# Kernel tuning notes

Measured on AMD Instinct MI355X. Metric: run time of the kernel, lower is better.

The kernel has to match this reference:

```python
import jax, jax.numpy as jnp
import numpy as np
from jax import lax


def ternarize(w):
    # TWN-style ternarization: threshold delta = 0.7*mean|w|, scale alpha =
    # mean |w| over surviving entries; straight-through in backward.
    aw = jnp.abs(w)
    delta = 0.7 * jnp.mean(aw)
    mask = (aw > delta).astype(w.dtype)
    alpha = jnp.sum(aw * mask) / jnp.maximum(jnp.sum(mask), 1.0)
    q = alpha * jnp.sign(w) * mask
    return w + lax.stop_gradient(q - w)


def conv2d(x, w, b):
    # x: [N,C,H,W], w: [O,I,kh,kw]
    y = lax.conv_general_dilated(x, w, window_strides=(1, 1), padding='VALID',
                                 dimension_numbers=('NCHW', 'OIHW', 'NCHW'))
    return y + b[None, :, None, None]


def maxpool2(x):
    return lax.reduce_window(x, -jnp.inf, lax.max,
                             window_dimensions=(1, 1, 2, 2),
                             window_strides=(1, 1, 2, 2), padding='VALID')


def setup_inputs() -> dict:
    key = jax.random.key(0)
    ks = jax.random.split(key, 11)
    n_classes = 10
    x = jax.random.normal(ks[0], (1024, 1, 32, 32), dtype=jnp.float32)
    # Kaiming-ish scaled params
    w1 = jax.random.normal(ks[1], (32, 1, 5, 5), jnp.float32) * (1.0 / np.sqrt(1 * 25))
    b1 = jnp.zeros((32,), jnp.float32)
    w2 = jax.random.normal(ks[2], (64, 32, 5, 5), jnp.float32) * (1.0 / np.sqrt(32 * 25))
    b2 = jnp.zeros((64,), jnp.float32)
    w3 = jax.random.normal(ks[3], (120, 64, 5, 5), jnp.float32) * (1.0 / np.sqrt(64 * 25))
    b3 = jnp.zeros((120,), jnp.float32)
    fw1 = jax.random.normal(ks[4], (84, 120), jnp.float32) * (1.0 / np.sqrt(120))
    fb1 = jnp.zeros((84,), jnp.float32)
    fw2 = jax.random.normal(ks[5], (n_classes, 84), jnp.float32) * (1.0 / np.sqrt(84))
    fb2 = jnp.zeros((n_classes,), jnp.float32)
    return {"x": x, "w1": w1, "b1": b1, "w2": w2, "b2": b2,
            "w3": w3, "b3": b3, "fw1": fw1, "fb1": fb1, "fw2": fw2, "fb2": fb2}


def reference(x, w1, b1, w2, b2, w3, b3, fw1, fb1, fw2, fb2):
    h = jnp.tanh(conv2d(x, ternarize(w1), b1))   # [N,32,28,28]
    h = maxpool2(h)                              # [N,32,14,14]
    h = jnp.tanh(conv2d(h, ternarize(w2), b2))   # [N,64,10,10]
    h = maxpool2(h)                              # [N,64,5,5]
    h = jnp.tanh(conv2d(h, ternarize(w3), b3))   # [N,120,1,1]
    h = h.reshape(h.shape[0], -1)                # [N,120]
    h = jnp.tanh(h @ ternarize(fw1).T + fb1)     # [N,84]
    logits = h @ ternarize(fw2).T + fb2          # [N,n_classes]
    probs = jax.nn.softmax(logits, axis=1)
    return (logits, probs)
```

## Files before the change

kernel.cpp:

```cpp
#include <hip/hip_runtime.h>
#include <hip/hip_bf16.h>
#include <math.h>


typedef __attribute__((ext_vector_type(8))) short bf16x8;
typedef __attribute__((ext_vector_type(4))) float f32x4;

static const size_t OFF_PB    = 0;
static const size_t OFF_Q1T   = 256;
static const size_t OFF_W2B   = 1056;
static const size_t OFF_W3B   = 26656;
static const size_t OFF_FW1T  = 129056;
static const size_t OFF_FW2T  = 139136;
static const size_t OFF_P2B   = 139976;
static const size_t OFF_H3    = 959176;

#define BPT 16

__device__ __forceinline__ ushort f2bf(float v) {
    unsigned u = __float_as_uint(v);
    unsigned r = (u + 0x7FFFu + ((u >> 16) & 1u)) >> 16;
    return (ushort)r;
}

__device__ __forceinline__ float tanh_fast(float x) {
    float e = __expf(-2.0f * fabsf(x));
    float r = 1.0f - 2.0f * e / (1.0f + e);
    return copysignf(r, x);
}

__device__ __forceinline__ void tensor_select(int tensor,
        const float* w1, const float* w2, const float* w3,
        const float* fw1, const float* fw2,
        const float*& src, int& O, int& K) {
    switch (tensor) {
        case 0: src = w1;  O = 32;  K = 25;   break;
        case 1: src = w2;  O = 64;  K = 800;  break;
        case 2: src = w3;  O = 120; K = 1600; break;
        case 3: src = fw1; O = 84;  K = 120;  break;
        default: src = fw2; O = 10; K = 84;   break;
    }
}

__device__ __forceinline__ float block_sum_256(float v, float* sbuf) {
    #pragma unroll
    for (int off = 32; off > 0; off >>= 1) v += __shfl_down(v, off);
    const int wid = threadIdx.x >> 6;
    if ((threadIdx.x & 63) == 0) sbuf[wid] = v;
    __syncthreads();
    return sbuf[0] + sbuf[1] + sbuf[2] + sbuf[3];
}

__device__ __forceinline__ float alpha_of(const float* pb, int tensor) {
    float s1 = 0.f, c = 0.f;
    #pragma unroll
    for (int i = 0; i < BPT; ++i) {
        s1 += pb[80 + tensor * BPT + i];
        c  += pb[160 + tensor * BPT + i];
    }
    return s1 / fmaxf(c, 1.0f);
}

__global__ __launch_bounds__(256)
void tern_pass1(const float* w1, const float* w2, const float* w3,
                const float* fw1, const float* fw2, float* pb) {
    __shared__ float sbuf[4];
    const int tensor = blockIdx.x / BPT;
    const int blk    = blockIdx.x % BPT;
    const float* src; int O, K;
    tensor_select(tensor, w1, w2, w3, fw1, fw2, src, O, K);
    const int n = O * K;
    float s = 0.f;
    for (int i = blk * 256 + threadIdx.x; i < n; i += BPT * 256)
        s += fabsf(src[i]);
    s = block_sum_256(s, sbuf);
    if (threadIdx.x == 0) pb[tensor * BPT + blk] = s;
}

__global__ __launch_bounds__(256)
void tern_pass2(const float* w1, const float* w2, const float* w3,
                const float* fw1, const float* fw2,
                float* q1t, ushort* w2b, ushort* w3b,
                float* fw1t, float* fw2t, float* pb) {
    __shared__ float sbuf[4];
    const int tensor = blockIdx.x / BPT;
    const int blk    = blockIdx.x % BPT;
    const float* src; int O, K;
    tensor_select(tensor, w1, w2, w3, fw1, fw2, src, O, K);
    const int n = O * K;
    float tot = 0.f;
    #pragma unroll
    for (int i = 0; i < BPT; ++i) tot += pb[tensor * BPT + i];
    const float delta = 0.7f * tot / (float)n;

    const ushort BP = 0x3F80u, BN = 0xBF80u;
    float s1 = 0.f, cnt = 0.f;

    if (tensor == 2) {
        for (int i = blk * 256 + threadIdx.x; i < 128 * 1600; i += BPT * 256) {
            ushort qb = 0;
            if (i < n) {
                float w = src[i];
                float aw = fabsf(w);
                if (aw > delta) { s1 += aw; cnt += 1.f; qb = (w > 0.f) ? BP : BN; }
            }
            w3b[i] = qb;
        }
    } else if (tensor == 1) {
        for (int i = blk * 256 + threadIdx.x; i < n; i += BPT * 256) {
            float w = src[i];
            float aw = fabsf(w);
            ushort qb = 0;
            if (aw > delta) { s1 += aw; cnt += 1.f; qb = (w > 0.f) ? BP : BN; }
            int oc = i / 800;
            int r  = i - oc * 800;
            int ic = r / 25;
            int tap = r - ic * 25;
            w2b[oc * 800 + tap * 32 + ic] = qb;
        }
    } else {
        float* dst = (tensor == 0) ? q1t : (tensor == 3) ? fw1t : fw2t;
        for (int i = blk * 256 + threadIdx.x; i < n; i += BPT * 256) {
            float w = src[i];
            float aw = fabsf(w);
            float q = 0.f;
            if (aw > delta) { s1 += aw; cnt += 1.f; q = (w > 0.f) ? 1.f : -1.f; }
            int o = i / K;
            int k = i - o * K;
            dst[k * O + o] = q;
        }
    }
    s1 = block_sum_256(s1, sbuf);
    __syncthreads();
    cnt = block_sum_256(cnt, sbuf);
    if (threadIdx.x == 0) {
        pb[80 + tensor * BPT + blk]  = s1;
        pb[160 + tensor * BPT + blk] = cnt;
    }
}

template<int TBASE, int TCNT>
__device__ __forceinline__ void conv2_phase(
        const ushort* __restrict__ w2b, const ushort* sxt,
        int n0, int mt0, int lane, f32x4 acc[4][2]) {
    const int col = lane & 15, quad = lane >> 4;
    bf16x8 bfr[TCNT][2];
    #pragma unroll
    for (int i = 0; i < TCNT; ++i) {
        const int tap = TBASE + i;
        #pragma unroll
        for (int np = 0; np < 2; ++np) {
            const int oc = n0 + np * 16 + col;
            bfr[i][np] = *(const bf16x8*)(w2b + (oc * 25 + tap) * 32 + quad * 8);
        }
    }
    #pragma unroll
    for (int mi = 0; mi < 4; ++mi) {
        int m = (mt0 + mi) * 16 + col;
        m = m < 100 ? m : 99;
        const int oh = m / 10, ow = m - oh * 10;
        const ushort* abase = sxt + (oh * 14 + ow) * 40 + quad * 8;
        #pragma unroll
        for (int i = 0; i < TCNT; ++i) {
            const int tap = TBASE + i;
            const int kh = tap / 5, kw = tap - kh * 5;
            bf16x8 af = *(const bf16x8*)(abase + (kh * 14 + kw) * 40);
            acc[mi][0] = __builtin_amdgcn_mfma_f32_16x16x32_bf16(af, bfr[i][0], acc[mi][0], 0, 0, 0);
            acc[mi][1] = __builtin_amdgcn_mfma_f32_16x16x32_bf16(af, bfr[i][1], acc[mi][1], 0, 0, 0);
        }
    }
}

__global__ __launch_bounds__(256)
void conv12_kernel(const float* __restrict__ x, const float* __restrict__ q1t,
                   const float* __restrict__ b1, const ushort* __restrict__ w2b,
                   const float* __restrict__ b2, const float* __restrict__ pb,
                   ushort* __restrict__ p2b) {
    __shared__ __align__(16) ushort sxt[196 * 40];
    __shared__ __align__(16) float hbuf[64 * 50];
    __shared__ float salpha[2];
    float* sx = hbuf;
    float* sw = hbuf + 1024;

    const int n = blockIdx.x;
    const int t = threadIdx.x;
    {
        const float4* src = (const float4*)(x + (size_t)n * 1024);
        if (t < 256) ((float4*)sx)[t] = src[t];
        if (t < 200) ((float4*)sw)[t] = ((const float4*)q1t)[t];
        if (t == 0) salpha[0] = alpha_of(pb, 0);
        if (t == 1) salpha[1] = alpha_of(pb, 1);
    }
    __syncthreads();

    const float a1 = salpha[0];
    const int ocg  = t >> 5;
    const int pos0 = t & 31;
    float bias[4];
    #pragma unroll
    for (int o = 0; o < 4; ++o) bias[o] = b1[ocg * 4 + o];

    for (int pos = pos0; pos < 196; pos += 32) {
        const int ph = pos / 14, pw = pos - ph * 14;
        const int r0 = 2 * ph, c0 = 2 * pw;
        float acc[4][4] = {};
        const float4* wp = (const float4*)sw + ocg;
        #pragma unroll
        for (int kh = 0; kh < 5; ++kh) {
            const float* xr = sx + (r0 + kh) * 32 + c0;
            float2 pa0 = *(const float2*)&xr[0];
            float2 pa1 = *(const float2*)&xr[2];
            float2 pa2 = *(const float2*)&xr[4];
            float2 pb0 = *(const float2*)&xr[32];
            float2 pb1 = *(const float2*)&xr[34];
            float2 pb2 = *(const float2*)&xr[36];
            const float xa[6] = {pa0.x, pa0.y, pa1.x, pa1.y, pa2.x, pa2.y};
            const float xb[6] = {pb0.x, pb0.y, pb1.x, pb1.y, pb2.x, pb2.y};
            #pragma unroll
            for (int kw = 0; kw < 5; ++kw) {
                const float4 w4 = *wp; wp += 8;
                const float x00 = xa[kw], x01 = xa[kw + 1];
                const float x10 = xb[kw], x11 = xb[kw + 1];
                acc[0][0] = fmaf(w4.x, x00, acc[0][0]);
                acc[0][1] = fmaf(w4.x, x01, acc[0][1]);
                acc[0][2] = fmaf(w4.x, x10, acc[0][2]);
                acc[0][3] = fmaf(w4.x, x11, acc[0][3]);
                acc[1][0] = fmaf(w4.y, x00, acc[1][0]);
                acc[1][1] = fmaf(w4.y, x01, acc[1][1]);
                acc[1][2] = fmaf(w4.y, x10, acc[1][2]);
                acc[1][3] = fmaf(w4.y, x11, acc[1][3]);
                acc[2][0] = fmaf(w4.z, x00, acc[2][0]);
                acc[2][1] = fmaf(w4.z, x01, acc[2][1]);
                acc[2][2] = fmaf(w4.z, x10, acc[2][2]);
                acc[2][3] = fmaf(w4.z, x11, acc[2][3]);
                acc[3][0] = fmaf(w4.w, x00, acc[3][0]);
                acc[3][1] = fmaf(w4.w, x01, acc[3][1]);
                acc[3][2] = fmaf(w4.w, x10, acc[3][2]);
                acc[3][3] = fmaf(w4.w, x11, acc[3][3]);
            }
        }
        ushort4 qv;
        {
            float m0 = fmaxf(fmaxf(acc[0][0], acc[0][1]), fmaxf(acc[0][2], acc[0][3]));
            float m1 = fmaxf(fmaxf(acc[1][0], acc[1][1]), fmaxf(acc[1][2], acc[1][3]));
            float m2 = fmaxf(fmaxf(acc[2][0], acc[2][1]), fmaxf(acc[2][2], acc[2][3]));
            float m3 = fmaxf(fmaxf(acc[3][0], acc[3][1]), fmaxf(acc[3][2], acc[3][3]));
            qv.x = f2bf(tanh_fast(fmaf(a1, m0, bias[0])));
            qv.y = f2bf(tanh_fast(fmaf(a1, m1, bias[1])));
            qv.z = f2bf(tanh_fast(fmaf(a1, m2, bias[2])));
            qv.w = f2bf(tanh_fast(fmaf(a1, m3, bias[3])));
        }
        *(ushort4*)(&sxt[pos * 40 + ocg * 4]) = qv;
    }
    __syncthreads();

    const int wave = t >> 6, lane = t & 63;
    const int n0  = (wave & 1) * 32;
    const int mt0 = (wave >> 1) * 4;
    f32x4 acc2[4][2] = {};
    conv2_phase<0, 13>(w2b, sxt, n0, mt0, lane, acc2);
    conv2_phase<13, 12>(w2b, sxt, n0, mt0, lane, acc2);

    {
        const int col = lane & 15, quad = lane >> 4;
        #pragma unroll
        for (int mi = 0; mi < 4; ++mi) {
            const int mrow = (mt0 + mi) * 16 + quad * 4;
            if (mrow < 100) {
                #pragma unroll
                for (int np = 0; np < 2; ++np) {
                    const int oc = n0 + np * 16 + col;
                    float2 hm;
                    hm.x = fmaxf(acc2[mi][np][0], acc2[mi][np][1]);
                    hm.y = fmaxf(acc2[mi][np][2], acc2[mi][np][3]);
                    *(float2*)(&hbuf[oc * 50 + (mrow >> 1)]) = hm;
                }
            }
        }
    }
    __syncthreads();

    const float a2 = salpha[1];
    for (int idx = t; idx < 1600; idx += 256) {
        const int oc = idx / 25, r = idx - oc * 25;
        const int ph = r / 5, pw = r - ph * 5;
        const float* hb = &hbuf[oc * 50 + ph * 10 + pw];
        float m = fmaxf(hb[0], hb[5]);
        p2b[(size_t)n * 1600 + idx] = f2bf(tanh_fast(fmaf(a2, m, b2[oc])));
    }
}

template<int STEPS>
__device__ __forceinline__ void conv3_chunk(const ushort* Abase, const ushort* B0,
                                            const ushort* B1, f32x4& acc0, f32x4& acc1) {
    #pragma unroll
    for (int s = 0; s < STEPS; ++s) {
        bf16x8 af = *(const bf16x8*)(Abase + s * 32);
        bf16x8 b0 = *(const bf16x8*)(B0 + s * 32);
        bf16x8 b1 = *(const bf16x8*)(B1 + s * 32);
        acc0 = __builtin_amdgcn_mfma_f32_16x16x32_bf16(af, b0, acc0, 0, 0, 0);
        acc1 = __builtin_amdgcn_mfma_f32_16x16x32_bf16(af, b1, acc1, 0, 0, 0);
    }
}

__global__ __launch_bounds__(256)
void conv3_mfma(const ushort* __restrict__ p2b, const ushort* __restrict__ w3b,
                const float* __restrict__ b3, const float* __restrict__ pb,
                float* __restrict__ h3) {
    __shared__ float red[4][64][8];
    __shared__ float salpha;
    const int t = threadIdx.x;
    const int wave = t >> 6, lane = t & 63;
    const int mt = blockIdx.x >> 2;
    const int npair = blockIdx.x & 3;
    const int col = lane & 15, quad = lane >> 4;
    const int kstart = (wave < 2) ? wave * 13 : 26 + (wave - 2) * 12;

    if (t == 0) salpha = alpha_of(pb, 2);

    const ushort* Abase = p2b + (size_t)(mt * 16 + col) * 1600 + kstart * 32 + quad * 8;
    const ushort* B0 = w3b + (size_t)(npair * 32 + col) * 1600 + kstart * 32 + quad * 8;
    const ushort* B1 = B0 + 16 * 1600;

    f32x4 acc0 = {}, acc1 = {};
    if (wave < 2) conv3_chunk<13>(Abase, B0, B1, acc0, acc1);
    else          conv3_chunk<12>(Abase, B0, B1, acc0, acc1);

    #pragma unroll
    for (int r = 0; r < 4; ++r) {
        red[wave][lane][r]     = acc0[r];
        red[wave][lane][4 + r] = acc1[r];
    }
    __syncthreads();

    {
        const float a3 = salpha;
        const int l = t & 63, vh = t >> 6;
        const int lcol = l & 15, lquad = l >> 4;
        const int img = mt * 16 + lquad * 4 + vh;
        #pragma unroll
        for (int j = 0; j < 2; ++j) {
            const int v = j * 4 + vh;
            float s = red[0][l][v] + red[1][l][v] + red[2][l][v] + red[3][l][v];
            const int oc = npair * 32 + j * 16 + lcol;
            if (oc < 120) h3[(size_t)img * 120 + oc] = tanh_fast(fmaf(a3, s, b3[oc]));
        }
    }
}

__global__ __launch_bounds__(128)
void fc_kernel(const float* __restrict__ h3, const float* __restrict__ fw1t,
               const float* __restrict__ fb1, const float* __restrict__ fw2t,
               const float* __restrict__ fb2, const float* __restrict__ pb,
               float* __restrict__ out) {
    const int n = blockIdx.x;
    __shared__ float sh[120];
    __shared__ float sh4[84];
    __shared__ float sl[10];
    __shared__ float salpha[2];
    const int t = threadIdx.x;
    if (t < 120) sh[t] = h3[(size_t)n * 120 + t];
    if (t == 120) salpha[0] = alpha_of(pb, 3);
    if (t == 121) salpha[1] = alpha_of(pb, 4);
    __syncthreads();
    if (t < 84) {
        const float af1 = salpha[0];
        float a = 0.f;
        #pragma unroll 4
        for (int k = 0; k < 120; ++k) a = fmaf(fw1t[k * 84 + t], sh[k], a);
        sh4[t] = tanh_fast(fmaf(af1, a, fb1[t]));
    }
    __syncthreads();
    if (t < 10) {
        const float af2 = salpha[1];
        float a = 0.f;
        #pragma unroll 4
        for (int k = 0; k < 84; ++k) a = fmaf(fw2t[k * 10 + t], sh4[k], a);
        const float lg = fmaf(af2, a, fb2[t]);
        sl[t] = lg;
        out[(size_t)n * 10 + t] = lg;
    }
    __syncthreads();
    if (t < 10) {
        float m = -INFINITY;
        #pragma unroll
        for (int i = 0; i < 10; ++i) m = fmaxf(m, sl[i]);
        float s = 0.f;
        #pragma unroll
        for (int i = 0; i < 10; ++i) s += expf(sl[i] - m);
        out[10240 + (size_t)n * 10 + t] = expf(sl[t] - m) / s;
    }
}

extern "C" void kernel_launch(void* const* d_in, const int* in_sizes, int n_in,
                              void* d_out, int out_size, void* d_ws, size_t ws_size,
                              hipStream_t stream) {
    const float* x   = (const float*)d_in[0];
    const float* w1  = (const float*)d_in[1];
    const float* b1  = (const float*)d_in[2];
    const float* w2  = (const float*)d_in[3];
    const float* b2  = (const float*)d_in[4];
    const float* w3  = (const float*)d_in[5];
    const float* b3  = (const float*)d_in[6];
    const float* fw1 = (const float*)d_in[7];
    const float* fb1 = (const float*)d_in[8];
    const float* fw2 = (const float*)d_in[9];
    const float* fb2 = (const float*)d_in[10];

    float* ws = (float*)d_ws;
    float*  pb   = ws + OFF_PB;
    float*  q1t  = ws + OFF_Q1T;
    ushort* w2b  = (ushort*)(ws + OFF_W2B);
    ushort* w3b  = (ushort*)(ws + OFF_W3B);
    float*  fw1t = ws + OFF_FW1T;
    float*  fw2t = ws + OFF_FW2T;
    ushort* p2b  = (ushort*)(ws + OFF_P2B);
    float*  h3   = ws + OFF_H3;
    float*  out  = (float*)d_out;

    tern_pass1<<<5 * BPT, 256, 0, stream>>>(w1, w2, w3, fw1, fw2, pb);
    tern_pass2<<<5 * BPT, 256, 0, stream>>>(w1, w2, w3, fw1, fw2,
                                            q1t, w2b, w3b, fw1t, fw2t, pb);
    conv12_kernel<<<1024, 256, 0, stream>>>(x, q1t, b1, w2b, b2, pb, p2b);
    conv3_mfma<<<256, 256, 0, stream>>>(p2b, w3b, b3, pb, h3);
    fc_kernel<<<1024, 128, 0, stream>>>(h3, fw1t, fb1, fw2t, fb2, pb, out);
}
```

Before: 163.2 us.

## Move conv1 onto bf16 MFMA via shared-memory im2col with padded ternary weights

Conv1 changes from scalar fp32 FMAs in registers to bf16 MFMA 16x16x32. The input image is converted to bf16 and an im2col matrix (25 taps padded to 32) is built in shared memory in two halves, and ternary w1 is stored as padded bf16 sign values. The horizontal part of the 2x2 pool is taken from the MFMA accumulator lanes and the vertical part in a later pass before tanh. Shared memory per block grows to about 53KB, which can cut occupancy, and the input is now rounded to bf16, which loses precision.

```diff
diff --git a/kernel.cpp b/kernel.cpp
--- a/kernel.cpp
+++ b/kernel.cpp
@@ -7,7 +7,7 @@
 typedef __attribute__((ext_vector_type(4))) float f32x4;
 
 static const size_t OFF_PB    = 0;
-static const size_t OFF_Q1T   = 256;
+static const size_t OFF_W1B   = 256;
 static const size_t OFF_W2B   = 1056;
 static const size_t OFF_W3B   = 26656;
 static const size_t OFF_FW1T  = 129056;
@@ -21,6 +21,9 @@
     unsigned u = __float_as_uint(v);
     unsigned r = (u + 0x7FFFu + ((u >> 16) & 1u)) >> 16;
     return (ushort)r;
+}
+__device__ __forceinline__ float bf2f(ushort h) {
+    return __uint_as_float((unsigned)h << 16);
 }
 
 __device__ __forceinline__ float tanh_fast(float x) {
@@ -80,7 +83,7 @@
 __global__ __launch_bounds__(256)
 void tern_pass2(const float* w1, const float* w2, const float* w3,
                 const float* fw1, const float* fw2,
-                float* q1t, ushort* w2b, ushort* w3b,
+                ushort* w1b, ushort* w2b, ushort* w3b,
                 float* fw1t, float* fw2t, float* pb) {
     __shared__ float sbuf[4];
     const int tensor = blockIdx.x / BPT;
@@ -96,7 +99,18 @@
     const ushort BP = 0x3F80u, BN = 0xBF80u;
     float s1 = 0.f, cnt = 0.f;
 
-    if (tensor == 2) {
+    if (tensor == 0) {
+        for (int j = blk * 256 + threadIdx.x; j < 1024; j += BPT * 256) {
+            const int oc = j >> 5, kk = j & 31;
+            ushort qb = 0;
+            if (kk < 25) {
+                float w = src[oc * 25 + kk];
+                float aw = fabsf(w);
+                if (aw > delta) { s1 += aw; cnt += 1.f; qb = (w > 0.f) ? BP : BN; }
+            }
+            w1b[j] = qb;
+        }
+    } else if (tensor == 2) {
         for (int i = blk * 256 + threadIdx.x; i < 128 * 1600; i += BPT * 256) {
             ushort qb = 0;
             if (i < n) {
@@ -119,7 +133,7 @@
             w2b[oc * 800 + tap * 32 + ic] = qb;
         }
     } else {
-        float* dst = (tensor == 0) ? q1t : (tensor == 3) ? fw1t : fw2t;
+        float* dst = (tensor == 3) ? fw1t : fw2t;
         for (int i = blk * 256 + threadIdx.x; i < n; i += BPT * 256) {
             float w = src[i];
             float aw = fabsf(w);
@@ -172,89 +186,96 @@
 }
 
 __global__ __launch_bounds__(256)
-void conv12_kernel(const float* __restrict__ x, const float* __restrict__ q1t,
+void conv12_kernel(const float* __restrict__ x, const ushort* __restrict__ w1b,
                    const float* __restrict__ b1, const ushort* __restrict__ w2b,
                    const float* __restrict__ b2, const float* __restrict__ pb,
                    ushort* __restrict__ p2b) {
-    __shared__ __align__(16) ushort sxt[196 * 40];
-    __shared__ __align__(16) float hbuf[64 * 50];
-    __shared__ float salpha[2];
-    float* sx = hbuf;
-    float* sw = hbuf + 1024;
+    __shared__ __align__(16) char smem[53008];
+    ushort* sxb    = (ushort*)smem;
+    ushort* A      = (ushort*)(smem + 2048);
+    ushort* sxt    = (ushort*)(smem + 2048);
+    ushort* hb1    = (ushort*)(smem + 27648);
+    float*  hb2    = (float*) (smem + 27648);
+    float*  sbias  = (float*) (smem + 52864);
+    float*  salpha = (float*) (smem + 52992);
 
     const int n = blockIdx.x;
     const int t = threadIdx.x;
+    const int wave = t >> 6, lane = t & 63;
+    const int col = lane & 15, quad = lane >> 4;
+
+    bf16x8 B0 = *(const bf16x8*)(w1b + col * 32 + quad * 8);
+    bf16x8 B1 = *(const bf16x8*)(w1b + (col + 16) * 32 + quad * 8);
+
     {
-        const float4* src = (const float4*)(x + (size_t)n * 1024);
-        if (t < 256) ((float4*)sx)[t] = src[t];
-        if (t < 200) ((float4*)sw)[t] = ((const float4*)q1t)[t];
-        if (t == 0) salpha[0] = alpha_of(pb, 0);
-        if (t == 1) salpha[1] = alpha_of(pb, 1);
-    }
-    __syncthreads();
-
-    const float a1 = salpha[0];
-    const int ocg  = t >> 5;
-    const int pos0 = t & 31;
-    float bias[4];
-    #pragma unroll
-    for (int o = 0; o < 4; ++o) bias[o] = b1[ocg * 4 + o];
-
-    for (int pos = pos0; pos < 196; pos += 32) {
-        const int ph = pos / 14, pw = pos - ph * 14;
-        const int r0 = 2 * ph, c0 = 2 * pw;
-        float acc[4][4] = {};
-        const float4* wp = (const float4*)sw + ocg;
-        #pragma unroll
-        for (int kh = 0; kh < 5; ++kh) {
-            const float* xr = sx + (r0 + kh) * 32 + c0;
-            float2 pa0 = *(const float2*)&xr[0];
-            float2 pa1 = *(const float2*)&xr[2];
-            float2 pa2 = *(const float2*)&xr[4];
-            float2 pb0 = *(const float2*)&xr[32];
-            float2 pb1 = *(const float2*)&xr[34];
-            float2 pb2 = *(const float2*)&xr[36];
-            const float xa[6] = {pa0.x, pa0.y, pa1.x, pa1.y, pa2.x, pa2.y};
-            const float xb[6] = {pb0.x, pb0.y, pb1.x, pb1.y, pb2.x, pb2.y};
+        float4 v = ((const float4*)(x + (size_t)n * 1024))[t];
+        ushort4 q;
+        q.x = f2bf(v.x); q.y = f2bf(v.y); q.z = f2bf(v.z); q.w = f2bf(v.w);
+        *(ushort4*)(sxb + t * 4) = q;
+        if (t < 32) sbias[t] = b1[t];
+        if (t == 32) salpha[0] = alpha_of(pb, 0);
+        if (t == 33) salpha[1] = alpha_of(pb, 1);
+    }
+    __syncthreads();
+
+    for (int half = 0; half < 2; ++half) {
+        const int base   = half ? 400 : 0;
+        const int rows   = half ? 384 : 400;
+        const int ntiles = half ? 24  : 25;
+
+        for (int p = base + t; p < base + rows; p += 256) {
+            const int pl = p - base;
+            const int oh = p / 28, ow = p % 28;
+            ushort v[25];
             #pragma unroll
-            for (int kw = 0; kw < 5; ++kw) {
-                const float4 w4 = *wp; wp += 8;
-                const float x00 = xa[kw], x01 = xa[kw + 1];
-                const float x10 = xb[kw], x11 = xb[kw + 1];
-                acc[0][0] = fmaf(w4.x, x00, acc[0][0]);
-                acc[0][1] = fmaf(w4.x, x01, acc[0][1]);
-                acc[0][2] = fmaf(w4.x, x10, acc[0][2]);
-                acc[0][3] = fmaf(w4.x, x11, acc[0][3]);
-                acc[1][0] = fmaf(w4.y, x00, acc[1][0]);
-                acc[1][1] = fmaf(w4.y, x01, acc[1][1]);
-                acc[1][2] = fmaf(w4.y, x10, acc[1][2]);
-                acc[1][3] = fmaf(w4.y, x11, acc[1][3]);
-                acc[2][0] = fmaf(w4.z, x00, acc[2][0]);
-                acc[2][1] = fmaf(w4.z, x01, acc[2][1]);
-                acc[2][2] = fmaf(w4.z, x10, acc[2][2]);
-                acc[2][3] = fmaf(w4.z, x11, acc[2][3]);
-                acc[3][0] = fmaf(w4.w, x00, acc[3][0]);
-                acc[3][1] = fmaf(w4.w, x01, acc[3][1]);
-                acc[3][2] = fmaf(w4.w, x10, acc[3][2]);
-                acc[3][3] = fmaf(w4.w, x11, acc[3][3]);
+            for (int kh = 0; kh < 5; ++kh) {
+                const ushort* r = sxb + (oh + kh) * 32 + ow;
+                v[kh * 5 + 0] = r[0]; v[kh * 5 + 1] = r[1]; v[kh * 5 + 2] = r[2];
+                v[kh * 5 + 3] = r[3]; v[kh * 5 + 4] = r[4];
             }
-        }
-        ushort4 qv;
-        {
-            float m0 = fmaxf(fmaxf(acc[0][0], acc[0][1]), fmaxf(acc[0][2], acc[0][3]));
-            float m1 = fmaxf(fmaxf(acc[1][0], acc[1][1]), fmaxf(acc[1][2], acc[1][3]));
-            float m2 = fmaxf(fmaxf(acc[2][0], acc[2][1]), fmaxf(acc[2][2], acc[2][3]));
-            float m3 = fmaxf(fmaxf(acc[3][0], acc[3][1]), fmaxf(acc[3][2], acc[3][3]));
-            qv.x = f2bf(tanh_fast(fmaf(a1, m0, bias[0])));
-            qv.y = f2bf(tanh_fast(fmaf(a1, m1, bias[1])));
-            qv.z = f2bf(tanh_fast(fmaf(a1, m2, bias[2])));
-            qv.w = f2bf(tanh_fast(fmaf(a1, m3, bias[3])));
-        }
-        *(ushort4*)(&sxt[pos * 40 + ocg * 4]) = qv;
-    }
-    __syncthreads();
-
-    const int wave = t >> 6, lane = t & 63;
+            unsigned d[16];
+            #pragma unroll
+            for (int j = 0; j < 12; ++j)
+                d[j] = (unsigned)v[2 * j] | ((unsigned)v[2 * j + 1] << 16);
+            d[12] = (unsigned)v[24];
+            d[13] = 0u; d[14] = 0u; d[15] = 0u;
+            uint4* arow = (uint4*)(A + pl * 32);
+            uint4 w0; w0.x = d[0];  w0.y = d[1];  w0.z = d[2];  w0.w = d[3];
+            uint4 w1; w1.x = d[4];  w1.y = d[5];  w1.z = d[6];  w1.w = d[7];
+            uint4 w2; w2.x = d[8];  w2.y = d[9];  w2.z = d[10]; w2.w = d[11];
+            uint4 w3; w3.x = d[12]; w3.y = d[13]; w3.z = d[14]; w3.w = d[15];
+            arow[0] = w0; arow[1] = w1; arow[2] = w2; arow[3] = w3;
+        }
+        __syncthreads();
+
+        for (int tile = wave; tile < ntiles; tile += 4) {
+            bf16x8 af = *(const bf16x8*)(A + (tile * 16 + col) * 32 + quad * 8);
+            f32x4 z = {};
+            f32x4 c0 = __builtin_amdgcn_mfma_f32_16x16x32_bf16(af, B0, z, 0, 0, 0);
+            f32x4 c1 = __builtin_amdgcn_mfma_f32_16x16x32_bf16(af, B1, z, 0, 0, 0);
+            const int p = base + tile * 16 + quad * 4;
+            const int oh = p / 28, ow2 = (p % 28) >> 1;
+            ushort2 h0, h1;
+            h0.x = f2bf(fmaxf(c0[0], c0[1])); h0.y = f2bf(fmaxf(c0[2], c0[3]));
+            h1.x = f2bf(fmaxf(c1[0], c1[1])); h1.y = f2bf(fmaxf(c1[2], c1[3]));
+            *(ushort2*)(hb1 + col * 394 + oh * 14 + ow2) = h0;
+            *(ushort2*)(hb1 + (col + 16) * 394 + oh * 14 + ow2) = h1;
+        }
+        __syncthreads();
+    }
+
+    {
+        const float a1 = salpha[0];
+        for (int idx = t; idx < 6272; idx += 256) {
+            const int oc = idx & 31, pos = idx >> 5;
+            const int ph = pos / 14, pw = pos - ph * 14;
+            const ushort* hp = hb1 + oc * 394 + (2 * ph) * 14 + pw;
+            float m = fmaxf(bf2f(hp[0]), bf2f(hp[14]));
+            sxt[pos * 40 + oc] = f2bf(tanh_fast(fmaf(a1, m, sbias[oc])));
+        }
+    }
+    __syncthreads();
+
     const int n0  = (wave & 1) * 32;
     const int mt0 = (wave >> 1) * 4;
     f32x4 acc2[4][2] = {};
@@ -262,7 +283,6 @@
     conv2_phase<13, 12>(w2b, sxt, n0, mt0, lane, acc2);
 
     {
-        const int col = lane & 15, quad = lane >> 4;
         #pragma unroll
         for (int mi = 0; mi < 4; ++mi) {
             const int mrow = (mt0 + mi) * 16 + quad * 4;
@@ -273,7 +293,7 @@
                     float2 hm;
                     hm.x = fmaxf(acc2[mi][np][0], acc2[mi][np][1]);
                     hm.y = fmaxf(acc2[mi][np][2], acc2[mi][np][3]);
-                    *(float2*)(&hbuf[oc * 50 + (mrow >> 1)]) = hm;
+                    *(float2*)(&hb2[oc * 50 + (mrow >> 1)]) = hm;
                 }
             }
         }
@@ -284,7 +304,7 @@
     for (int idx = t; idx < 1600; idx += 256) {
         const int oc = idx / 25, r = idx - oc * 25;
         const int ph = r / 5, pw = r - ph * 5;
-        const float* hb = &hbuf[oc * 50 + ph * 10 + pw];
+        const float* hb = &hb2[oc * 50 + ph * 10 + pw];
         float m = fmaxf(hb[0], hb[5]);
         p2b[(size_t)n * 1600 + idx] = f2bf(tanh_fast(fmaf(a2, m, b2[oc])));
     }
@@ -409,7 +429,7 @@
 
     float* ws = (float*)d_ws;
     float*  pb   = ws + OFF_PB;
-    float*  q1t  = ws + OFF_Q1T;
+    ushort* w1b  = (ushort*)(ws + OFF_W1B);
     ushort* w2b  = (ushort*)(ws + OFF_W2B);
     ushort* w3b  = (ushort*)(ws + OFF_W3B);
     float*  fw1t = ws + OFF_FW1T;
@@ -420,8 +440,8 @@
 
     tern_pass1<<<5 * BPT, 256, 0, stream>>>(w1, w2, w3, fw1, fw2, pb);
     tern_pass2<<<5 * BPT, 256, 0, stream>>>(w1, w2, w3, fw1, fw2,
-                                            q1t, w2b, w3b, fw1t, fw2t, pb);
-    conv12_kernel<<<1024, 256, 0, stream>>>(x, q1t, b1, w2b, b2, pb, p2b);
+                                            w1b, w2b, w3b, fw1t, fw2t, pb);
+    conv12_kernel<<<1024, 256, 0, stream>>>(x, w1b, b1, w2b, b2, pb, p2b);
     conv3_mfma<<<256, 256, 0, stream>>>(p2b, w3b, b3, pb, h3);
     fc_kernel<<<1024, 128, 0, stream>>>(h3, fw1t, fb1, fw2t, fb2, pb, out);
 }
```

Result: no change. 163.5 us (+0.2%).
